# Kernel optimization log

Measured on AMD Instinct MI355X. Metric: run time of the kernel, lower is better.

## Reference

```python
import jax, jax.numpy as jnp
import numpy as np

DEG = 7
RANK = 8
B = 2_000_000

def setup_inputs() -> dict:
    key = jax.random.key(0)
    k_x, k0, k1, k2, k3 = jax.random.split(key, 5)
    d1 = DEG + 1
    # xavier_normal std = sqrt(2 / (fan_in + fan_out)); for 3D cores torch uses
    # fan_in = rank*(deg+1) style flattening, but any gaussian init is fine for a
    # numerical reference; use std matching 2D xavier on the (first, last) dims.
    def xavier(k, shape):
        fan_in, fan_out = shape[0], shape[-1]
        std = np.sqrt(2.0 / (fan_in + fan_out))
        return jax.random.normal(k, shape, dtype=jnp.float32) * std
    return {
        "X": jax.random.normal(k_x, (B, 4), dtype=jnp.float32),
        "G0": xavier(k0, (d1, RANK)),
        "G1": xavier(k1, (RANK, d1, RANK)),
        "G2": xavier(k2, (RANK, d1, RANK)),
        "G3": xavier(k3, (RANK, d1)),
    }

def reference(X, G0, G1, G2, G3):
    # poly bases: P[b, dim, p] = X[b, dim] ** p, p = 0..deg
    exps = jnp.arange(DEG + 1)               # [d1]
    P = X[:, :, None] ** exps                # [B, 4, d1]
    # chained TT contraction, left to right (avoids any large intermediate)
    t = jnp.einsum('bd,dr->br', P[:, 0], G0)           # [B, r]
    t = jnp.einsum('br,rds,bd->bs', t, G1, P[:, 1])    # [B, r]
    t = jnp.einsum('bs,sdt,bd->bt', t, G2, P[:, 2])    # [B, r]
    res = jnp.einsum('bt,td,bd->b', t, G3, P[:, 3])    # [B]
    return res.reshape(-1, 1)
```

## Files before the change

### kernel.cpp

```cpp
#include <hip/hip_runtime.h>
#include <hip/hip_bf16.h>

typedef float f32x4 __attribute__((ext_vector_type(4)));
typedef short bf16x8 __attribute__((ext_vector_type(8)));

__device__ inline unsigned cvt_pk_bf16(float a, float b) {
    unsigned r;
    asm("v_cvt_pk_bf16_f32 %0, %1, %2" : "=v"(r) : "v"(a), "v"(b));
    return r;
}
union FragU { unsigned u[4]; bf16x8 v; };

__device__ inline bf16x8 pack8(const float f[8]) {
    FragU x;
    x.u[0] = cvt_pk_bf16(f[0], f[1]);
    x.u[1] = cvt_pk_bf16(f[2], f[3]);
    x.u[2] = cvt_pk_bf16(f[4], f[5]);
    x.u[3] = cvt_pk_bf16(f[6], f[7]);
    return x.v;
}

__device__ inline bf16x8 splat8(float v) {
    FragU x;
    unsigned p = cvt_pk_bf16(v, v);
    x.u[0] = p; x.u[1] = p; x.u[2] = p; x.u[3] = p;
    return x.v;
}

__device__ inline void build_b(const float* __restrict__ G, int col, int grp,
                               bf16x8* Bh, bf16x8* Bl) {
    #pragma unroll
    for (int q = 0; q < 2; ++q) {
        FragU hi, lo;
        #pragma unroll
        for (int pr = 0; pr < 4; ++pr) {
            float v0 = 0.f, v1 = 0.f;
            if (col < 8) {
                v0 = G[(32*q + 8*grp + 2*pr    ) * 8 + col];
                v1 = G[(32*q + 8*grp + 2*pr + 1) * 8 + col];
            }
            float h0 = __bfloat162float(__float2bfloat16(v0));
            float h1 = __bfloat162float(__float2bfloat16(v1));
            hi.u[pr] = cvt_pk_bf16(h0, h1);
            lo.u[pr] = cvt_pk_bf16(v0 - h0, v1 - h1);
        }
        Bh[q] = hi.v;
        Bl[q] = lo.v;
    }
}

#define POWERS(p, xx)                                              \
    p[0] = 1.f;  p[1] = (xx);      p[2] = p[1]*p[1];               \
    p[3] = p[2]*p[1]; p[4] = p[2]*p[2]; p[5] = p[4]*p[1];          \
    p[6] = p[4]*p[2]; p[7] = p[4]*p[3];

#define ROWW 12

__global__ __launch_bounds__(256) void tt_poly_kernel(
    const float* __restrict__ X,
    const float* __restrict__ G0,
    const float* __restrict__ G1,
    const float* __restrict__ G2,
    const float* __restrict__ G3,
    float* __restrict__ out,
    int B, int NW)
{
    __shared__ float L[4][3][64 * ROWW];

    const int tid  = threadIdx.x;
    const int w    = tid >> 6;
    const int lane = tid & 63;
    const int col  = lane & 15;
    const int grp  = lane >> 4;

    int rowLbl[4], colLbl[4];
    {
        bf16x8 ones = splat8(1.f);
        bf16x8 lbl  = splat8((float)col);
        f32x4 pr = {0.f, 0.f, 0.f, 0.f};
        f32x4 pc = {0.f, 0.f, 0.f, 0.f};
        pr = __builtin_amdgcn_mfma_f32_16x16x32_bf16(lbl, ones, pr, 0, 0, 0);
        pc = __builtin_amdgcn_mfma_f32_16x16x32_bf16(ones, lbl, pc, 0, 0, 0);
        #pragma unroll
        for (int j = 0; j < 4; ++j) {
            rowLbl[j] = (int)(pr[j] * 0.03125f + 0.5f);
            colLbl[j] = (int)(pc[j] * 0.03125f + 0.5f);
        }
    }

    bf16x8 B1h[2], B1l[2], B2h[2], B2l[2];
    build_b(G1, col, grp, B1h, B1l);
    build_b(G2, col, grp, B2h, B2l);

    float* T0 = &L[w][0][0];
    float* T1 = &L[w][1][0];
    float* T2 = &L[w][2][0];
    const int gw = blockIdx.x * 4 + w;

    #pragma unroll 1
    for (int it = 0; it < 4; ++it) {
        const int b = (it * NW + gw) * 64 + lane;
        float4 xv = make_float4(0.f, 0.f, 0.f, 0.f);
        if (b < B) xv = reinterpret_cast<const float4*>(X)[b];

        {
            float p[8];
            POWERS(p, xv.x)
            f32x4 tlo, thi;
            #pragma unroll
            for (int r = 0; r < 4; ++r) {
                float ta = 0.f, tb = 0.f;
                #pragma unroll
                for (int d = 0; d < 8; ++d) {
                    ta = fmaf(p[d], G0[d*8 + r    ], ta);
                    tb = fmaf(p[d], G0[d*8 + r + 4], tb);
                }
                tlo[r] = ta; thi[r] = tb;
            }
            *reinterpret_cast<f32x4*>(&T0[lane*ROWW    ]) = tlo;
            *reinterpret_cast<f32x4*>(&T0[lane*ROWW + 4]) = thi;
            *reinterpret_cast<float2*>(&T0[lane*ROWW + 8]) = make_float2(xv.y, xv.z);
        }
        __syncthreads();

        #pragma unroll
        for (int g4 = 0; g4 < 4; ++g4) {
            const int base = (g4*16 + col) * ROWW;
            float ta = T0[base + grp];
            float tb = T0[base + grp + 4];
            float x1 = T0[base + 8];
            float p[8];
            POWERS(p, x1)
            float f0[8], f1[8];
            #pragma unroll
            for (int e = 0; e < 8; ++e) { f0[e] = ta*p[e]; f1[e] = tb*p[e]; }
            bf16x8 a0 = pack8(f0), a1 = pack8(f1);
            f32x4 acc = {0.f, 0.f, 0.f, 0.f};
            acc = __builtin_amdgcn_mfma_f32_16x16x32_bf16(a0, B1h[0], acc, 0, 0, 0);
            acc = __builtin_amdgcn_mfma_f32_16x16x32_bf16(a0, B1l[0], acc, 0, 0, 0);
            acc = __builtin_amdgcn_mfma_f32_16x16x32_bf16(a1, B1h[1], acc, 0, 0, 0);
            acc = __builtin_amdgcn_mfma_f32_16x16x32_bf16(a1, B1l[1], acc, 0, 0, 0);
            #pragma unroll
            for (int j = 0; j < 4; ++j)
                if (colLbl[j] < 8)
                    T1[(g4*16 + rowLbl[j])*ROWW + colLbl[j]] = acc[j];
        }
        __syncthreads();

        #pragma unroll
        for (int g4 = 0; g4 < 4; ++g4) {
            const int base = (g4*16 + col) * ROWW;
            float tc = T1[base + grp];
            float td = T1[base + grp + 4];
            float x2 = T0[base + 9];
            float p[8];
            POWERS(p, x2)
            float f0[8], f1[8];
            #pragma unroll
            for (int e = 0; e < 8; ++e) { f0[e] = tc*p[e]; f1[e] = td*p[e]; }
            bf16x8 a0 = pack8(f0), a1 = pack8(f1);
            f32x4 acc = {0.f, 0.f, 0.f, 0.f};
            acc = __builtin_amdgcn_mfma_f32_16x16x32_bf16(a0, B2h[0], acc, 0, 0, 0);
            acc = __builtin_amdgcn_mfma_f32_16x16x32_bf16(a0, B2l[0], acc, 0, 0, 0);
            acc = __builtin_amdgcn_mfma_f32_16x16x32_bf16(a1, B2h[1], acc, 0, 0, 0);
            acc = __builtin_amdgcn_mfma_f32_16x16x32_bf16(a1, B2l[1], acc, 0, 0, 0);
            #pragma unroll
            for (int j = 0; j < 4; ++j)
                if (colLbl[j] < 8)
                    T2[(g4*16 + rowLbl[j])*ROWW + colLbl[j]] = acc[j];
        }
        __syncthreads();

        {
            f32x4 u0 = *reinterpret_cast<const f32x4*>(&T2[lane*ROWW    ]);
            f32x4 u1 = *reinterpret_cast<const f32x4*>(&T2[lane*ROWW + 4]);
            float p[8];
            POWERS(p, xv.w)
            float res = 0.f;
            #pragma unroll
            for (int t8 = 0; t8 < 8; ++t8) {
                float wt = G3[t8*8];
                #pragma unroll
                for (int d = 1; d < 8; ++d)
                    wt = fmaf(p[d], G3[t8*8 + d], wt);
                float tv = (t8 < 4) ? u0[t8] : u1[t8 - 4];
                res = fmaf(tv, wt, res);
            }
            if (b < B) out[b] = res;
        }
    }
}

extern "C" void kernel_launch(void* const* d_in, const int* in_sizes, int n_in,
                              void* d_out, int out_size, void* d_ws, size_t ws_size,
                              hipStream_t stream) {
    const float* X  = (const float*)d_in[0];
    const float* G0 = (const float*)d_in[1];
    const float* G1 = (const float*)d_in[2];
    const float* G2 = (const float*)d_in[3];
    const float* G3 = (const float*)d_in[4];
    float* out = (float*)d_out;

    int B = in_sizes[0] / 4;
    int block = 256;
    int grid = (B + 1023) / 1024;
    int NW = grid * 4;
    tt_poly_kernel<<<grid, block, 0, stream>>>(X, G0, G1, G2, G3, out, B, NW);
}
```

Baseline: 42.01 us.

## Replace block barriers with wave-local LDS fences and interleave rank slots

Each wave works only on its own LDS slice, so the block-wide __syncthreads are replaced by a per-wave s_waitcnt lgkmcnt(0) plus a scheduling barrier. This removes cross-wave stalls. The rank dimension in LDS is also permuted so that the two values each lane needs sit next to each other, letting one float2 read replace two scalar reads. The final contraction remaps slots back to rank indices. Dropping the barrier relies on lockstep execution within a wave for LDS visibility.

```diff
diff --git a/kernel.cpp b/kernel.cpp
--- a/kernel.cpp
+++ b/kernel.cpp
@@ -25,6 +25,11 @@
     unsigned p = cvt_pk_bf16(v, v);
     x.u[0] = p; x.u[1] = p; x.u[2] = p; x.u[3] = p;
     return x.v;
+}
+
+__device__ inline void wave_fence() {
+    asm volatile("s_waitcnt lgkmcnt(0)" ::: "memory");
+    __builtin_amdgcn_sched_barrier(0);
 }
 
 __device__ inline void build_b(const float* __restrict__ G, int col, int grp,
@@ -73,7 +78,7 @@
     const int col  = lane & 15;
     const int grp  = lane >> 4;
 
-    int rowLbl[4], colLbl[4];
+    int rowLbl[4], slotLbl[4], colOk[4];
     {
         bf16x8 ones = splat8(1.f);
         bf16x8 lbl  = splat8((float)col);
@@ -84,7 +89,9 @@
         #pragma unroll
         for (int j = 0; j < 4; ++j) {
             rowLbl[j] = (int)(pr[j] * 0.03125f + 0.5f);
-            colLbl[j] = (int)(pc[j] * 0.03125f + 0.5f);
+            int c     = (int)(pc[j] * 0.03125f + 0.5f);
+            colOk[j]  = (c < 8);
+            slotLbl[j] = 2 * (c & 3) + ((c >> 2) & 1);
         }
     }
 
@@ -106,34 +113,33 @@
         {
             float p[8];
             POWERS(p, xv.x)
-            f32x4 tlo, thi;
-            #pragma unroll
-            for (int r = 0; r < 4; ++r) {
-                float ta = 0.f, tb = 0.f;
+            float t[8];
+            #pragma unroll
+            for (int r = 0; r < 8; ++r) {
+                float a = 0.f;
                 #pragma unroll
-                for (int d = 0; d < 8; ++d) {
-                    ta = fmaf(p[d], G0[d*8 + r    ], ta);
-                    tb = fmaf(p[d], G0[d*8 + r + 4], tb);
-                }
-                tlo[r] = ta; thi[r] = tb;
+                for (int d = 0; d < 8; ++d)
+                    a = fmaf(p[d], G0[d*8 + r], a);
+                t[r] = a;
             }
-            *reinterpret_cast<f32x4*>(&T0[lane*ROWW    ]) = tlo;
-            *reinterpret_cast<f32x4*>(&T0[lane*ROWW + 4]) = thi;
+            f32x4 v0 = {t[0], t[4], t[1], t[5]};
+            f32x4 v1 = {t[2], t[6], t[3], t[7]};
+            *reinterpret_cast<f32x4*>(&T0[lane*ROWW    ]) = v0;
+            *reinterpret_cast<f32x4*>(&T0[lane*ROWW + 4]) = v1;
             *reinterpret_cast<float2*>(&T0[lane*ROWW + 8]) = make_float2(xv.y, xv.z);
         }
-        __syncthreads();
+        wave_fence();
 
         #pragma unroll
         for (int g4 = 0; g4 < 4; ++g4) {
             const int base = (g4*16 + col) * ROWW;
-            float ta = T0[base + grp];
-            float tb = T0[base + grp + 4];
-            float x1 = T0[base + 8];
+            float2 tp = *reinterpret_cast<const float2*>(&T0[base + 2*grp]);
+            float x1  = T0[base + 8];
             float p[8];
             POWERS(p, x1)
             float f0[8], f1[8];
             #pragma unroll
-            for (int e = 0; e < 8; ++e) { f0[e] = ta*p[e]; f1[e] = tb*p[e]; }
+            for (int e = 0; e < 8; ++e) { f0[e] = tp.x*p[e]; f1[e] = tp.y*p[e]; }
             bf16x8 a0 = pack8(f0), a1 = pack8(f1);
             f32x4 acc = {0.f, 0.f, 0.f, 0.f};
             acc = __builtin_amdgcn_mfma_f32_16x16x32_bf16(a0, B1h[0], acc, 0, 0, 0);
@@ -142,22 +148,21 @@
             acc = __builtin_amdgcn_mfma_f32_16x16x32_bf16(a1, B1l[1], acc, 0, 0, 0);
             #pragma unroll
             for (int j = 0; j < 4; ++j)
-                if (colLbl[j] < 8)
-                    T1[(g4*16 + rowLbl[j])*ROWW + colLbl[j]] = acc[j];
-        }
-        __syncthreads();
+                if (colOk[j])
+                    T1[(g4*16 + rowLbl[j])*ROWW + slotLbl[j]] = acc[j];
+        }
+        wave_fence();
 
         #pragma unroll
         for (int g4 = 0; g4 < 4; ++g4) {
             const int base = (g4*16 + col) * ROWW;
-            float tc = T1[base + grp];
-            float td = T1[base + grp + 4];
-            float x2 = T0[base + 9];
+            float2 tp = *reinterpret_cast<const float2*>(&T1[base + 2*grp]);
+            float x2  = T0[base + 9];
             float p[8];
             POWERS(p, x2)
             float f0[8], f1[8];
             #pragma unroll
-            for (int e = 0; e < 8; ++e) { f0[e] = tc*p[e]; f1[e] = td*p[e]; }
+            for (int e = 0; e < 8; ++e) { f0[e] = tp.x*p[e]; f1[e] = tp.y*p[e]; }
             bf16x8 a0 = pack8(f0), a1 = pack8(f1);
             f32x4 acc = {0.f, 0.f, 0.f, 0.f};
             acc = __builtin_amdgcn_mfma_f32_16x16x32_bf16(a0, B2h[0], acc, 0, 0, 0);
@@ -166,24 +171,26 @@
             acc = __builtin_amdgcn_mfma_f32_16x16x32_bf16(a1, B2l[1], acc, 0, 0, 0);
             #pragma unroll
             for (int j = 0; j < 4; ++j)
-                if (colLbl[j] < 8)
-                    T2[(g4*16 + rowLbl[j])*ROWW + colLbl[j]] = acc[j];
-        }
-        __syncthreads();
+                if (colOk[j])
+                    T2[(g4*16 + rowLbl[j])*ROWW + slotLbl[j]] = acc[j];
+        }
+        wave_fence();
 
         {
             f32x4 u0 = *reinterpret_cast<const f32x4*>(&T2[lane*ROWW    ]);
             f32x4 u1 = *reinterpret_cast<const f32x4*>(&T2[lane*ROWW + 4]);
+            const int tmap[8] = {0, 4, 1, 5, 2, 6, 3, 7};
             float p[8];
             POWERS(p, xv.w)
             float res = 0.f;
             #pragma unroll
-            for (int t8 = 0; t8 < 8; ++t8) {
+            for (int sl = 0; sl < 8; ++sl) {
+                const int t8 = tmap[sl];
                 float wt = G3[t8*8];
                 #pragma unroll
                 for (int d = 1; d < 8; ++d)
                     wt = fmaf(p[d], G3[t8*8 + d], wt);
-                float tv = (t8 < 4) ? u0[t8] : u1[t8 - 4];
+                float tv = (sl < 4) ? u0[sl] : u1[sl - 4];
                 res = fmaf(tv, wt, res);
             }
             if (b < B) out[b] = res;
```

After: 40.37 us. 3.9% less time.
